# Kernel tuning notes

Measured on AMD Instinct MI355X. Metric: run time of the kernel, lower is better.

## Reference

```python
import jax, jax.numpy as jnp
import numpy as np

B, T, C = 4, 2048, 2048
H = 16
D = C // H  # 128


def setup_inputs() -> dict:
    key = jax.random.key(0)
    ks = jax.random.split(key, 9)
    s = 0.02
    return {
        "x": jax.random.normal(ks[0], (B, T, C), dtype=jnp.float32),
        "wq": jax.random.normal(ks[1], (C, C), dtype=jnp.float32) * s,
        "bq": jax.random.normal(ks[2], (C,), dtype=jnp.float32) * s,
        "wk": jax.random.normal(ks[3], (C, C), dtype=jnp.float32) * s,
        "bk": jax.random.normal(ks[4], (C,), dtype=jnp.float32) * s,
        "wv": jax.random.normal(ks[5], (C, C), dtype=jnp.float32) * s,
        "bv": jax.random.normal(ks[6], (C,), dtype=jnp.float32) * s,
        "wo": jax.random.normal(ks[7], (C, C), dtype=jnp.float32) * s,
        "bo": jax.random.normal(ks[8], (C,), dtype=jnp.float32) * s,
    }


def reference(x, wq, bq, wk, bk, wv, bv, wo, bo):
    Bz, Tz, Cz = x.shape
    # projections (torch Linear: x @ W^T + b)
    q = (x @ wq.T + bq).reshape(Bz, Tz, H, D).transpose(0, 2, 1, 3)  # [B,H,T,D]
    k = (x @ wk.T + bk).reshape(Bz, Tz, H, D).transpose(0, 2, 1, 3)
    v = (x @ wv.T + bv).reshape(Bz, Tz, H, D).transpose(0, 2, 1, 3)
    scale = 1.0 / jnp.sqrt(jnp.float32(D))
    scores = jnp.einsum("bhqd,bhkd->bhqk", q, k) * scale  # [B,H,T,T]
    causal = jnp.tril(jnp.ones((Tz, Tz), dtype=bool))
    scores = jnp.where(causal, scores, jnp.float32(-jnp.inf))
    att = jax.nn.softmax(scores, axis=-1)
    out = jnp.einsum("bhqk,bhkd->bhqd", att, v)  # [B,H,T,D]
    out = out.transpose(0, 2, 1, 3).reshape(Bz, Tz, Cz)
    out = out @ wo.T + bo
    return out
```

## Files before the change

kernel.cpp:

```cpp
#include <hip/hip_runtime.h>
#include <hip/hip_bf16.h>

typedef float  f32x4  __attribute__((ext_vector_type(4)));
typedef __bf16 bf16x8 __attribute__((ext_vector_type(8)));
typedef __bf16 bf16x4 __attribute__((ext_vector_type(4)));

#define Bz 4
#define Tz 2048
#define Cz 2048
#define Hh 16
#define Dd 128
#define Mm 8192

__device__ __forceinline__ void gload_lds16(const __bf16* g, __bf16* l) {
  __builtin_amdgcn_global_load_lds(
      (const __attribute__((address_space(1))) void*)g,
      (__attribute__((address_space(3))) void*)l, 16, 0, 0);
}

__global__ __launch_bounds__(256)
void cvt_bf16(const float* __restrict__ in, __bf16* __restrict__ out, int n8) {
  int i = blockIdx.x * 256 + threadIdx.x;
  if (i >= n8) return;
  size_t base = (size_t)i * 8;
  f32x4 a = *(const f32x4*)(in + base);
  f32x4 b = *(const f32x4*)(in + base + 4);
  bf16x8 o;
  o[0]=(__bf16)a[0]; o[1]=(__bf16)a[1]; o[2]=(__bf16)a[2]; o[3]=(__bf16)a[3];
  o[4]=(__bf16)b[0]; o[5]=(__bf16)b[1]; o[6]=(__bf16)b[2]; o[7]=(__bf16)b[3];
  *(bf16x8*)(out + base) = o;
}

template<int MODE>
__global__ __launch_bounds__(256, 2)
void gemm_bt(const __bf16* __restrict__ A, const __bf16* __restrict__ W,
             const float* __restrict__ bias, void* __restrict__ Out,
             int K, float scale)
{
  __shared__ __bf16 As[128 * 64];
  __shared__ __bf16 Bs[128 * 64];

  const int tid  = threadIdx.x;
  const int lane = tid & 63;
  const int wave = tid >> 6;
  const int wm = wave >> 1, wn = wave & 1;
  const int g  = lane >> 4;
  const int lr = lane & 15;
  const int row0 = blockIdx.x * 128;
  const int col0 = blockIdx.y * 128;

  const int srow = lane >> 3;
  const int sblk = lane & 7;

  f32x4 acc[4][4] = {};

  for (int kt = 0; kt < K; kt += 64) {
    __syncthreads();
    #pragma unroll
    for (int p = 0; p < 4; ++p) {
      const int rb = p * 32 + wave * 8;
      const int r  = rb + srow;
      const int cb = sblk ^ (r & 7);
      gload_lds16(A + (size_t)(row0 + r) * K + kt + cb * 8, As + rb * 64);
      gload_lds16(W + (size_t)(col0 + r) * K + kt + cb * 8, Bs + rb * 64);
    }
    __syncthreads();
    #pragma unroll
    for (int kk = 0; kk < 2; ++kk) {
      bf16x8 af[4], bfr[4];
      #pragma unroll
      for (int i = 0; i < 4; ++i) {
        const int ar = wm * 64 + i * 16 + lr;
        af[i]  = *(const bf16x8*)(As + ar * 64 + ((((kk<<2)|g) ^ (ar & 7)) << 3));
        const int br = wn * 64 + i * 16 + lr;
        bfr[i] = *(const bf16x8*)(Bs + br * 64 + ((((kk<<2)|g) ^ (br & 7)) << 3));
      }
      #pragma unroll
      for (int i = 0; i < 4; ++i)
        #pragma unroll
        for (int j = 0; j < 4; ++j)
          acc[i][j] = __builtin_amdgcn_mfma_f32_16x16x32_bf16(af[i], bfr[j], acc[i][j], 0, 0, 0);
    }
  }

  #pragma unroll
  for (int j = 0; j < 4; ++j) {
    const int col = col0 + wn * 64 + j * 16 + lr;
    const float bv = bias[col];
    #pragma unroll
    for (int i = 0; i < 4; ++i) {
      if (MODE == 2) {
        const int row = row0 + wm * 64 + i * 16 + g * 4;
        const int b = row >> 11, t = row & (Tz - 1);
        const int h = col >> 7,  d = col & (Dd - 1);
        bf16x4 v4;
        #pragma unroll
        for (int r = 0; r < 4; ++r) v4[r] = (__bf16)(acc[i][j][r] + bv);
        *(bf16x4*)((__bf16*)Out + ((size_t)(b * Hh + h) * Dd + d) * Tz + t) = v4;
      } else {
        #pragma unroll
        for (int r = 0; r < 4; ++r) {
          const int row = row0 + wm * 64 + i * 16 + g * 4 + r;
          const float v = acc[i][j][r] + bv;
          if (MODE == 0) {
            const int b = row >> 11, t = row & (Tz - 1);
            const int h = col >> 7,  d = col & (Dd - 1);
            ((__bf16*)Out)[((size_t)(b * Hh + h) * Tz + t) * Dd + d] = (__bf16)(v * scale);
          } else {
            ((float*)Out)[(size_t)row * Cz + col] = v;
          }
        }
      }
    }
  }
}

__global__ __launch_bounds__(256, 2)
void attn_fwd(const __bf16* __restrict__ Q, const __bf16* __restrict__ Kg,
              const __bf16* __restrict__ Vt, __bf16* __restrict__ O)
{
  __shared__ __bf16 Ks[2][64 * 128];
  __shared__ __bf16 Vs[2][128 * 64];
  __shared__ __bf16 Ps[4][32 * 64];

  const int tid  = threadIdx.x;
  const int lane = tid & 63;
  const int wave = tid >> 6;
  const int g  = lane >> 4;
  const int lr = lane & 15;
  const int pair = blockIdx.y;
  const int b = pair >> 4, h = pair & 15;

  const __bf16* Qp = Q  + (size_t)pair * Tz * Dd;
  const __bf16* Kp = Kg + (size_t)pair * Tz * Dd;
  const __bf16* Vp = Vt + (size_t)pair * Dd * Tz;

  #define STAGE_KV(kv0_, buf_)                                                  \
    {                                                                           \
      const int kv0s = (kv0_);                                                  \
      _Pragma("unroll")                                                         \
      for (int p = 0; p < 4; ++p) {                                             \
        const int r  = p * 16 + wave * 4 + (lane >> 4);                         \
        const int cb = (lane & 15) ^ (r & 7);                                   \
        gload_lds16(Kp + (size_t)(kv0s + r) * Dd + cb * 8,                      \
                    &Ks[buf_][p * 2048 + wave * 512]);                          \
        const int d  = p * 32 + wave * 8 + (lane >> 3);                         \
        const int cv = (lane & 7) ^ (d & 7);                                    \
        gload_lds16(Vp + (size_t)d * Tz + kv0s + cv * 8,                        \
                    &Vs[buf_][p * 2048 + wave * 512]);                          \
      }                                                                         \
    }

  for (int pass = 0; pass < 2; ++pass) {
    const int qt  = pass == 0 ? (15 - (int)blockIdx.x) : (int)blockIdx.x;
    const int qw0 = qt * 128 + wave * 32;

    bf16x8 qf[2][4];
    #pragma unroll
    for (int im = 0; im < 2; ++im)
      #pragma unroll
      for (int ks = 0; ks < 4; ++ks)
        qf[im][ks] = *(const bf16x8*)(Qp + (size_t)(qw0 + im*16 + lr) * Dd + ks*32 + g*8);

    f32x4 oacc[2][8] = {};
    float mrow[2][4], lsum[2][4];
    #pragma unroll
    for (int im = 0; im < 2; ++im)
      #pragma unroll
      for (int r = 0; r < 4; ++r) { mrow[im][r] = -1e30f; lsum[im][r] = 0.f; }

    const int ntiles = 2 * qt + 2;

    STAGE_KV(0, 0);
    __syncthreads();

    for (int kt = 0; kt < ntiles; ++kt) {
      const int cur = kt & 1;
      const int kv0 = kt * 64;
      if (kt + 1 < ntiles) STAGE_KV((kt + 1) * 64, cur ^ 1);

      if (kv0 <= qw0 + 31) {
        f32x4 sacc[2][4] = {};
        __builtin_amdgcn_s_setprio(1);
        #pragma unroll
        for (int ks = 0; ks < 4; ++ks) {
          bf16x8 kf[4];
          #pragma unroll
          for (int in = 0; in < 4; ++in) {
            const int r = in*16 + lr;
            kf[in] = *(const bf16x8*)(&Ks[cur][r * 128 + ((((ks<<2)|g) ^ (r & 7)) << 3)]);
          }
          #pragma unroll
          for (int im = 0; im < 2; ++im)
            #pragma unroll
            for (int in = 0; in < 4; ++in)
              sacc[im][in] = __builtin_amdgcn_mfma_f32_16x16x32_bf16(qf[im][ks], kf[in], sacc[im][in], 0, 0, 0);
        }
        __builtin_amdgcn_s_setprio(0);
        if (kv0 + 63 > qw0) {
          #pragma unroll
          for (int im = 0; im < 2; ++im)
            #pragma unroll
            for (int in = 0; in < 4; ++in)
              #pragma unroll
              for (int r = 0; r < 4; ++r) {
                const int qrow = qw0 + im*16 + g*4 + r;
                const int kcol = kv0 + in*16 + lr;
                if (kcol > qrow) sacc[im][in][r] = -3e38f;
              }
        }
        #pragma unroll
        for (int im = 0; im < 2; ++im) {
          float pmax[4];
          #pragma unroll
          for (int r = 0; r < 4; ++r) {
            float m = fmaxf(fmaxf(sacc[im][0][r], sacc[im][1][r]),
                            fmaxf(sacc[im][2][r], sacc[im][3][r]));
            #pragma unroll
            for (int off = 1; off < 16; off <<= 1)
              m = fmaxf(m, __shfl_xor(m, off));
            pmax[r] = m;
          }
          bool need = false;
          #pragma unroll
          for (int r = 0; r < 4; ++r) need |= (pmax[r] > mrow[im][r] + 11.54f);
          if (__any(need)) {
            #pragma unroll
            for (int r = 0; r < 4; ++r) {
              const bool  up = pmax[r] > mrow[im][r] + 11.54f;
              const float mn = up ? pmax[r] : mrow[im][r];
              const float corr = exp2f(mrow[im][r] - mn);
              mrow[im][r] = mn;
              lsum[im][r] *= corr;
              #pragma unroll
              for (int dn = 0; dn < 8; ++dn)
                oacc[im][dn][r] *= corr;
            }
          }
          float rs[4] = {0.f, 0.f, 0.f, 0.f};
          #pragma unroll
          for (int in = 0; in < 4; ++in) {
            #pragma unroll
            for (int r = 0; r < 4; ++r) {
              const float pv = __builtin_amdgcn_exp2f(sacc[im][in][r] - mrow[im][r]);
              rs[r] += pv;
              const int row = im*16 + g*4 + r;
              const int col = in*16 + lr;
              Ps[wave][row * 64 + ((((col >> 3) ^ (row & 7)) << 3) | (col & 7))] = (__bf16)pv;
            }
          }
          #pragma unroll
          for (int r = 0; r < 4; ++r) {
            float s = rs[r];
            #pragma unroll
            for (int off = 1; off < 16; off <<= 1)
              s += __shfl_xor(s, off);
            lsum[im][r] += s;
          }
        }
        __builtin_amdgcn_s_setprio(1);
        #pragma unroll
        for (int kk = 0; kk < 2; ++kk) {
          bf16x8 pa[2];
          #pragma unroll
          for (int im = 0; im < 2; ++im) {
            const int row = im*16 + lr;
            pa[im] = *(const bf16x8*)(&Ps[wave][row * 64 + ((((kk<<2)|g) ^ (row & 7)) << 3)]);
          }
          #pragma unroll
          for (int dn = 0; dn < 8; ++dn) {
            const int d = dn*16 + lr;
            bf16x8 vb = *(const bf16x8*)(&Vs[cur][d * 64 + ((((kk<<2)|g) ^ (d & 7)) << 3)]);
            #pragma unroll
            for (int im = 0; im < 2; ++im)
              oacc[im][dn] = __builtin_amdgcn_mfma_f32_16x16x32_bf16(pa[im], vb, oacc[im][dn], 0, 0, 0);
          }
        }
        __builtin_amdgcn_s_setprio(0);
      }
      __syncthreads();
    }

    #pragma unroll
    for (int im = 0; im < 2; ++im)
      #pragma unroll
      for (int dn = 0; dn < 8; ++dn)
        #pragma unroll
        for (int r = 0; r < 4; ++r) {
          const int qrow = qw0 + im*16 + g*4 + r;
          const float v = oacc[im][dn][r] / lsum[im][r];
          O[((size_t)(b * Tz + qrow)) * Cz + h * Dd + dn*16 + lr] = (__bf16)v;
        }
  }
  #undef STAGE_KV
}

extern "C" void kernel_launch(void* const* d_in, const int* in_sizes, int n_in,
                              void* d_out, int out_size, void* d_ws, size_t ws_size,
                              hipStream_t stream) {
  const float* x  = (const float*)d_in[0];
  const float* wq = (const float*)d_in[1];
  const float* bq = (const float*)d_in[2];
  const float* wk = (const float*)d_in[3];
  const float* bk = (const float*)d_in[4];
  const float* wv = (const float*)d_in[5];
  const float* bv = (const float*)d_in[6];
  const float* wo = (const float*)d_in[7];
  const float* bo = (const float*)d_in[8];
  float* out = (float*)d_out;

  char* w = (char*)d_ws;
  __bf16* xb   = (__bf16*)w; w += (size_t)Mm * Cz * 2;
  __bf16* wbuf = (__bf16*)w; w += (size_t)Cz * Cz * 2;
  __bf16* qb   = (__bf16*)w; w += (size_t)Mm * Cz * 2;
  __bf16* kb   = (__bf16*)w; w += (size_t)Mm * Cz * 2;
  __bf16* vbuf = (__bf16*)w; w += (size_t)Mm * Cz * 2;
  if (ws_size < (size_t)(w - (char*)d_ws)) return;

  const int nx8 = Mm * Cz / 8;
  const int nw8 = Cz * Cz / 8;
  dim3 ggrid(Mm / 128, Cz / 128);
  const float qscale = 0.12752551286084110f;

  cvt_bf16<<<nx8 / 256, 256, 0, stream>>>(x, xb, nx8);

  cvt_bf16<<<nw8 / 256, 256, 0, stream>>>(wq, wbuf, nw8);
  gemm_bt<0><<<ggrid, 256, 0, stream>>>(xb, wbuf, bq, qb, Cz, qscale);

  cvt_bf16<<<nw8 / 256, 256, 0, stream>>>(wk, wbuf, nw8);
  gemm_bt<0><<<ggrid, 256, 0, stream>>>(xb, wbuf, bk, kb, Cz, 1.0f);

  cvt_bf16<<<nw8 / 256, 256, 0, stream>>>(wv, wbuf, nw8);
  gemm_bt<2><<<ggrid, 256, 0, stream>>>(xb, wbuf, bv, vbuf, Cz, 1.0f);

  __bf16* ob = xb;
  attn_fwd<<<dim3(8, Bz * Hh), 256, 0, stream>>>(qb, kb, vbuf, ob);

  cvt_bf16<<<nw8 / 256, 256, 0, stream>>>(wo, wbuf, nw8);
  gemm_bt<1><<<ggrid, 256, 0, stream>>>(ob, wbuf, bo, out, Cz, 1.0f);
}
```

Before: 454.0 us.

## Transpose QK^T MFMA so each lane owns one query row for softmax

Swaps the MFMA operands so the score tile is computed transposed, making each lane hold four kv columns of a single query row. Row max and row sum now need only two cross-lane shuffles instead of sixteen, and the per-row state drops to one scalar per lane. P is written to LDS as 4-wide vector stores with a new swizzle, and the correction and normalization factors are broadcast back to the output accumulator layout with shuffles. This cuts softmax shuffle and scalar work per tile, in exchange for extra broadcast shuffles on rescale and a more intricate swizzle that must match the PV reads.

```diff
diff --git a/kernel.cpp b/kernel.cpp
--- a/kernel.cpp
+++ b/kernel.cpp
@@ -163,11 +163,9 @@
         qf[im][ks] = *(const bf16x8*)(Qp + (size_t)(qw0 + im*16 + lr) * Dd + ks*32 + g*8);
 
     f32x4 oacc[2][8] = {};
-    float mrow[2][4], lsum[2][4];
-    #pragma unroll
-    for (int im = 0; im < 2; ++im)
-      #pragma unroll
-      for (int r = 0; r < 4; ++r) { mrow[im][r] = -1e30f; lsum[im][r] = 0.f; }
+    float mrow[2], lsum[2];
+    mrow[0] = mrow[1] = -1e30f;
+    lsum[0] = lsum[1] = 0.f;
 
     const int ntiles = 2 * qt + 2;
 
@@ -194,78 +192,82 @@
           for (int im = 0; im < 2; ++im)
             #pragma unroll
             for (int in = 0; in < 4; ++in)
-              sacc[im][in] = __builtin_amdgcn_mfma_f32_16x16x32_bf16(qf[im][ks], kf[in], sacc[im][in], 0, 0, 0);
+              sacc[im][in] = __builtin_amdgcn_mfma_f32_16x16x32_bf16(kf[in], qf[im][ks], sacc[im][in], 0, 0, 0);
         }
         __builtin_amdgcn_s_setprio(0);
+
         if (kv0 + 63 > qw0) {
           #pragma unroll
-          for (int im = 0; im < 2; ++im)
+          for (int im = 0; im < 2; ++im) {
+            const int q = qw0 + im*16 + lr;
             #pragma unroll
             for (int in = 0; in < 4; ++in)
               #pragma unroll
               for (int r = 0; r < 4; ++r) {
-                const int qrow = qw0 + im*16 + g*4 + r;
-                const int kcol = kv0 + in*16 + lr;
-                if (kcol > qrow) sacc[im][in][r] = -3e38f;
+                const int kv = kv0 + in*16 + g*4 + r;
+                if (kv > q) sacc[im][in][r] = -3e38f;
               }
-        }
+          }
+        }
+
         #pragma unroll
         for (int im = 0; im < 2; ++im) {
-          float pmax[4];
-          #pragma unroll
-          for (int r = 0; r < 4; ++r) {
-            float m = fmaxf(fmaxf(sacc[im][0][r], sacc[im][1][r]),
-                            fmaxf(sacc[im][2][r], sacc[im][3][r]));
+          float m = fmaxf(fmaxf(sacc[im][0][0], sacc[im][0][1]),
+                          fmaxf(sacc[im][0][2], sacc[im][0][3]));
+          #pragma unroll
+          for (int in = 1; in < 4; ++in)
+            m = fmaxf(m, fmaxf(fmaxf(sacc[im][in][0], sacc[im][in][1]),
+                               fmaxf(sacc[im][in][2], sacc[im][in][3])));
+          m = fmaxf(m, __shfl_xor(m, 16));
+          m = fmaxf(m, __shfl_xor(m, 32));
+
+          const bool need = m > mrow[im] + 11.54f;
+          if (__any(need)) {
+            const float mn   = need ? m : mrow[im];
+            const float corr = __builtin_amdgcn_exp2f(mrow[im] - mn);
+            mrow[im] = mn;
+            lsum[im] *= corr;
+            const int sb = 20 * g;
+            const float c0 = __shfl(corr, sb + 0);
+            const float c1 = __shfl(corr, sb + 1);
+            const float c2 = __shfl(corr, sb + 2);
+            const float c3 = __shfl(corr, sb + 3);
             #pragma unroll
-            for (int off = 1; off < 16; off <<= 1)
-              m = fmaxf(m, __shfl_xor(m, off));
-            pmax[r] = m;
-          }
-          bool need = false;
-          #pragma unroll
-          for (int r = 0; r < 4; ++r) need |= (pmax[r] > mrow[im][r] + 11.54f);
-          if (__any(need)) {
-            #pragma unroll
-            for (int r = 0; r < 4; ++r) {
-              const bool  up = pmax[r] > mrow[im][r] + 11.54f;
-              const float mn = up ? pmax[r] : mrow[im][r];
-              const float corr = exp2f(mrow[im][r] - mn);
-              mrow[im][r] = mn;
-              lsum[im][r] *= corr;
-              #pragma unroll
-              for (int dn = 0; dn < 8; ++dn)
-                oacc[im][dn][r] *= corr;
+            for (int dn = 0; dn < 8; ++dn) {
+              oacc[im][dn][0] *= c0; oacc[im][dn][1] *= c1;
+              oacc[im][dn][2] *= c2; oacc[im][dn][3] *= c3;
             }
           }
-          float rs[4] = {0.f, 0.f, 0.f, 0.f};
+
+          float rs = 0.f;
+          const int prow = im*16 + lr;
           #pragma unroll
           for (int in = 0; in < 4; ++in) {
-            #pragma unroll
-            for (int r = 0; r < 4; ++r) {
-              const float pv = __builtin_amdgcn_exp2f(sacc[im][in][r] - mrow[im][r]);
-              rs[r] += pv;
-              const int row = im*16 + g*4 + r;
-              const int col = in*16 + lr;
-              Ps[wave][row * 64 + ((((col >> 3) ^ (row & 7)) << 3) | (col & 7))] = (__bf16)pv;
-            }
-          }
-          #pragma unroll
-          for (int r = 0; r < 4; ++r) {
-            float s = rs[r];
-            #pragma unroll
-            for (int off = 1; off < 16; off <<= 1)
-              s += __shfl_xor(s, off);
-            lsum[im][r] += s;
-          }
-        }
+            const float p0 = __builtin_amdgcn_exp2f(sacc[im][in][0] - mrow[im]);
+            const float p1 = __builtin_amdgcn_exp2f(sacc[im][in][1] - mrow[im]);
+            const float p2 = __builtin_amdgcn_exp2f(sacc[im][in][2] - mrow[im]);
+            const float p3 = __builtin_amdgcn_exp2f(sacc[im][in][3] - mrow[im]);
+            rs += (p0 + p1) + (p2 + p3);
+            bf16x4 q4;
+            q4[0] = (__bf16)p0; q4[1] = (__bf16)p1;
+            q4[2] = (__bf16)p2; q4[3] = (__bf16)p3;
+            const int bs = (in*4 + g) ^ ((prow & 3) << 2);
+            *(bf16x4*)(&Ps[wave][prow * 64 + bs * 4]) = q4;
+          }
+          rs += __shfl_xor(rs, 16);
+          rs += __shfl_xor(rs, 32);
+          lsum[im] += rs;
+        }
+
         __builtin_amdgcn_s_setprio(1);
         #pragma unroll
         for (int kk = 0; kk < 2; ++kk) {
           bf16x8 pa[2];
           #pragma unroll
           for (int im = 0; im < 2; ++im) {
-            const int row = im*16 + lr;
-            pa[im] = *(const bf16x8*)(&Ps[wave][row * 64 + ((((kk<<2)|g) ^ (row & 7)) << 3)]);
+            const int prow = im*16 + lr;
+            const int bs = (kk*8 + 2*g) ^ ((prow & 3) << 2);
+            pa[im] = *(const bf16x8*)(&Ps[wave][prow * 64 + bs * 4]);
           }
           #pragma unroll
           for (int dn = 0; dn < 8; ++dn) {
@@ -282,15 +284,23 @@
     }
 
     #pragma unroll
-    for (int im = 0; im < 2; ++im)
+    for (int im = 0; im < 2; ++im) {
+      const float inv = 1.0f / lsum[im];
+      const int sb = 20 * g;
+      const float i0 = __shfl(inv, sb + 0);
+      const float i1 = __shfl(inv, sb + 1);
+      const float i2 = __shfl(inv, sb + 2);
+      const float i3 = __shfl(inv, sb + 3);
       #pragma unroll
-      for (int dn = 0; dn < 8; ++dn)
-        #pragma unroll
-        for (int r = 0; r < 4; ++r) {
-          const int qrow = qw0 + im*16 + g*4 + r;
-          const float v = oacc[im][dn][r] / lsum[im][r];
-          O[((size_t)(b * Tz + qrow)) * Cz + h * Dd + dn*16 + lr] = (__bf16)v;
-        }
+      for (int dn = 0; dn < 8; ++dn) {
+        const int qrow = qw0 + im*16 + g*4;
+        const int d    = h * Dd + dn*16 + lr;
+        O[((size_t)(b * Tz + qrow + 0)) * Cz + d] = (__bf16)(oacc[im][dn][0] * i0);
+        O[((size_t)(b * Tz + qrow + 1)) * Cz + d] = (__bf16)(oacc[im][dn][1] * i1);
+        O[((size_t)(b * Tz + qrow + 2)) * Cz + d] = (__bf16)(oacc[im][dn][2] * i2);
+        O[((size_t)(b * Tz + qrow + 3)) * Cz + d] = (__bf16)(oacc[im][dn][3] * i3);
+      }
+    }
   }
   #undef STAGE_KV
 }
```

Measured after the change: 412.3 us. 9.2% less time.
